# Kernel tuning notes

Hardware: AMD Instinct MI355X
Metric: run time of the kernel (lower is better)

Reference implementation:

```python
import jax, jax.numpy as jnp
import numpy as np

H = 16       # n_heads
DH = 32      # head_dim
LN_EPS = 1e-5


def setup_inputs() -> dict:
    key = jax.random.key(0)
    ks = jax.random.split(key, 10)
    B, N, D, CZ = 1, 768, 512, 128
    sc = 0.05
    return {
        "s": jax.random.normal(ks[0], (B, N, D), jnp.float32),
        "z": jax.random.normal(ks[1], (B, N, N, CZ), jnp.float32),
        "Wq": jax.random.normal(ks[2], (D, D), jnp.float32) * sc,
        "bq": jax.random.normal(ks[3], (D,), jnp.float32) * sc,
        "Wk": jax.random.normal(ks[4], (D, D), jnp.float32) * sc,
        "Wv": jax.random.normal(ks[5], (D, D), jnp.float32) * sc,
        "Wg": jax.random.normal(ks[6], (D, D), jnp.float32) * sc,
        "Wo": jax.random.normal(ks[7], (D, D), jnp.float32) * sc,
        "ln_w": jnp.ones((CZ,), jnp.float32),
        "ln_b": jnp.zeros((CZ,), jnp.float32),
        "Wz": jax.random.normal(ks[8], (H, CZ), jnp.float32) * sc,
    }


def _layernorm(x, w, b):
    mu = jnp.mean(x, axis=-1, keepdims=True)
    var = jnp.var(x, axis=-1, keepdims=True)
    return (x - mu) * jax.lax.rsqrt(var + LN_EPS) * w + b


def reference(s, z, Wq, bq, Wk, Wv, Wg, Wo, ln_w, ln_b, Wz):
    B, N, D = s.shape
    scale = DH ** -0.5
    # fused QKV projections (only q has a bias; k/v bias slots are zero)
    q = (s @ Wq.T + bq).reshape(B, N, H, DH)
    k = (s @ Wk.T).reshape(B, N, H, DH)
    v = (s @ Wv.T).reshape(B, N, H, DH)
    # pair bias: layernorm over c_z then linear c_z -> n_heads, permuted to [B,H,N,N]
    zb = _layernorm(z, ln_w, ln_b) @ Wz.T            # [B,N,N,H]
    bias = jnp.transpose(zb, (0, 3, 1, 2))            # [B,H,N,N]
    logits = jnp.einsum("bqhd,bkhd->bhqk", q, k) * scale + bias
    attn = jax.nn.softmax(logits, axis=-1)
    o = jnp.einsum("bhqk,bkhd->bqhd", attn, v).reshape(B, N, H * DH)
    # sigmoid gate, then output projection
    g = s @ Wg.T
    o = o * jax.nn.sigmoid(g)
    return o @ Wo.T
```

## Files before the change

### kernel.cpp

```cpp
#include <hip/hip_runtime.h>
#include <hip/hip_bf16.h>

#define N_TOK 768
#define D_MODEL 512
#define CZd 128
#define NH 16
#define DHd 32

__global__ __launch_bounds__(256) void bias_kernel(
    const float* __restrict__ z, const float* __restrict__ ln_w,
    const float* __restrict__ ln_b, const float* __restrict__ Wz,
    float* __restrict__ bias)
{
    __shared__ float sWz[NH * CZd];
    __shared__ float swb[2 * CZd];
    __shared__ __align__(16) float sbias[NH][68];
    int t = threadIdx.x;
    for (int i = t; i < NH * CZd; i += 256) sWz[i] = Wz[i];
    if (t < CZd) { swb[t] = ln_w[t]; swb[CZd + t] = ln_b[t]; }
    __syncthreads();

    int q   = blockIdx.y;
    int k0  = blockIdx.x * 64;
    int lane = t & 63;
    int wv   = t >> 6;
    int g    = lane >> 2;
    int sub  = lane & 3;
    int k    = k0 + wv * 16 + g;

    const float* zrow = z + ((size_t)q * N_TOK + k) * CZd;

    float vals[32];
    float sum = 0.f, sumsq = 0.f;
#pragma unroll
    for (int i = 0; i < 8; ++i) {
        float4 v4 = *(const float4*)(zrow + (sub + 4 * i) * 4);
        vals[4*i+0] = v4.x; vals[4*i+1] = v4.y;
        vals[4*i+2] = v4.z; vals[4*i+3] = v4.w;
        sum   += v4.x + v4.y + v4.z + v4.w;
        sumsq += v4.x*v4.x + v4.y*v4.y + v4.z*v4.z + v4.w*v4.w;
    }
    sum   += __shfl_xor(sum, 1);   sum   += __shfl_xor(sum, 2);
    sumsq += __shfl_xor(sumsq, 1); sumsq += __shfl_xor(sumsq, 2);

    float mu   = sum * (1.f / CZd);
    float var  = sumsq * (1.f / CZd) - mu * mu;
    float rstd = rsqrtf(var + 1e-5f);

#pragma unroll
    for (int i = 0; i < 8; ++i) {
#pragma unroll
        for (int jj = 0; jj < 4; ++jj) {
            int e = 16 * i + 4 * sub + jj;
            vals[4*i+jj] = (vals[4*i+jj] - mu) * rstd * swb[e] + swb[CZd + e];
        }
    }

#pragma unroll
    for (int h = 0; h < NH; ++h) {
        float p = 0.f;
#pragma unroll
        for (int i = 0; i < 8; ++i) {
#pragma unroll
            for (int jj = 0; jj < 4; ++jj) {
                int e = 16 * i + 4 * sub + jj;
                p += vals[4*i+jj] * sWz[h * CZd + e];
            }
        }
        p += __shfl_xor(p, 1); p += __shfl_xor(p, 2);
        if ((h & 3) == sub) sbias[h][wv * 16 + g] = p;
    }
    __syncthreads();

    {
        int h  = t >> 4;
        int c4 = t & 15;
        float4 v = *(const float4*)&sbias[h][c4 * 4];
        *(float4*)&bias[((size_t)h * N_TOK + q) * N_TOK + k0 + c4 * 4] = v;
    }
}

#define BKP 32

__global__ __launch_bounds__(256) void qkvg_kernel(
    const float* __restrict__ s,
    const float* __restrict__ Wq, const float* __restrict__ bq,
    const float* __restrict__ Wk, const float* __restrict__ Wv,
    const float* __restrict__ Wg, float* __restrict__ qkvg)
{
    __shared__ __align__(16) float As[BKP][68];
    __shared__ __align__(16) float Bs[BKP][68];
    int t  = threadIdx.x;
    int m0 = blockIdx.y * 64;
    int n0 = blockIdx.x * 64;
    int sel  = n0 >> 9;
    int nloc = n0 & 511;
    const float* W = (sel == 0) ? Wq : (sel == 1) ? Wk : (sel == 2) ? Wv : Wg;

    int tm = t >> 4, tn = t & 15;
    float acc[4][4] = {};

    for (int kt = 0; kt < 512; kt += BKP) {
#pragma unroll
        for (int i = 0; i < 2; ++i) {
            int idx = t + i * 256;
            int row = idx >> 3;
            int c4  = idx & 7;
            float4 a4 = *(const float4*)&s[(size_t)(m0 + row) * 512 + kt + c4 * 4];
            float4 b4 = *(const float4*)&W[(size_t)(nloc + row) * 512 + kt + c4 * 4];
            As[c4*4+0][row] = a4.x; As[c4*4+1][row] = a4.y;
            As[c4*4+2][row] = a4.z; As[c4*4+3][row] = a4.w;
            Bs[c4*4+0][row] = b4.x; Bs[c4*4+1][row] = b4.y;
            Bs[c4*4+2][row] = b4.z; Bs[c4*4+3][row] = b4.w;
        }
        __syncthreads();
#pragma unroll
        for (int kk = 0; kk < BKP; ++kk) {
            float4 a4 = *(const float4*)&As[kk][tm * 4];
            float4 b4 = *(const float4*)&Bs[kk][tn * 4];
            acc[0][0] += a4.x * b4.x; acc[0][1] += a4.x * b4.y;
            acc[0][2] += a4.x * b4.z; acc[0][3] += a4.x * b4.w;
            acc[1][0] += a4.y * b4.x; acc[1][1] += a4.y * b4.y;
            acc[1][2] += a4.y * b4.z; acc[1][3] += a4.y * b4.w;
            acc[2][0] += a4.z * b4.x; acc[2][1] += a4.z * b4.y;
            acc[2][2] += a4.z * b4.z; acc[2][3] += a4.z * b4.w;
            acc[3][0] += a4.w * b4.x; acc[3][1] += a4.w * b4.y;
            acc[3][2] += a4.w * b4.z; acc[3][3] += a4.w * b4.w;
        }
        __syncthreads();
    }

#pragma unroll
    for (int i = 0; i < 4; ++i) {
        int row = m0 + tm * 4 + i;
        float4 v;
        int colb = n0 + tn * 4;
        v.x = acc[i][0]; v.y = acc[i][1]; v.z = acc[i][2]; v.w = acc[i][3];
        if (sel == 0) {
            v.x += bq[colb + 0]; v.y += bq[colb + 1];
            v.z += bq[colb + 2]; v.w += bq[colb + 3];
        }
        *(float4*)&qkvg[(size_t)row * 2048 + colb] = v;
    }
}

#define QT 16
#define KT 64

__global__ __launch_bounds__(256) void attn_kernel(
    const float* __restrict__ qkvg, const float* __restrict__ bias,
    float* __restrict__ o_g)
{
    __shared__ float kt_s[KT][32];
    __shared__ float vt_s[KT][32];
    __shared__ __align__(16) float pt[QT][68];
    __shared__ float mrun[QT], lrun[QT], scalef[QT];

    int t  = threadIdx.x;
    int h  = blockIdx.y;
    int Q0 = blockIdx.x * QT;

    int qi_l = t >> 4;
    int c16  = t & 15;
    int d   = t & 31;
    int qg  = t >> 5;
    int qi0 = qg * 2, qi1 = qg * 2 + 1;

    float4 qreg[8];
    {
        const float* qrow = qkvg + (size_t)(Q0 + qi_l) * 2048 + h * 32;
#pragma unroll
        for (int j = 0; j < 8; ++j) qreg[j] = ((const float4*)qrow)[j];
    }

    float acc0 = 0.f, acc1 = 0.f;
    if (t < QT) { mrun[t] = -1e30f; lrun[t] = 0.f; }
    __syncthreads();

    const float scale = 0.17677669529663687f;

    for (int k0 = 0; k0 < N_TOK; k0 += KT) {
#pragma unroll
        for (int i = 0; i < 2; ++i) {
            int idx = t + i * 256;
            int row = idx >> 3;
            int c4  = idx & 7;
            const float* kp = qkvg + (size_t)(k0 + row) * 2048 +  512 + h * 32 + c4 * 4;
            const float* vp = qkvg + (size_t)(k0 + row) * 2048 + 1024 + h * 32 + c4 * 4;
            float4 k4 = *(const float4*)kp;
            float4 v4 = *(const float4*)vp;
            int sc4 = c4 ^ (row & 7);
            *(float4*)&kt_s[row][sc4 * 4] = k4;
            *(float4*)&vt_s[row][c4 * 4]  = v4;
        }
        __syncthreads();

#pragma unroll
        for (int j = 0; j < 4; ++j) {
            int kk = c16 + 16 * j;
            float dot = 0.f;
#pragma unroll
            for (int c4 = 0; c4 < 8; ++c4) {
                int sc4 = c4 ^ (kk & 7);
                float4 k4 = *(const float4*)&kt_s[kk][sc4 * 4];
                float4 q4 = qreg[c4];
                dot += k4.x*q4.x + k4.y*q4.y + k4.z*q4.z + k4.w*q4.w;
            }
            float b = bias[((size_t)h * N_TOK + (Q0 + qi_l)) * N_TOK + k0 + kk];
            pt[qi_l][kk] = dot * scale + b;
        }
        __syncthreads();

        {
            int lane = t & 63, w = t >> 6;
#pragma unroll
            for (int r4 = 0; r4 < 4; ++r4) {
                int r = w * 4 + r4;
                float x = pt[r][lane];
                float mx = x;
#pragma unroll
                for (int o = 32; o >= 1; o >>= 1) mx = fmaxf(mx, __shfl_xor(mx, o));
                float mold = mrun[r];
                float mnew = fmaxf(mold, mx);
                float p = __expf(x - mnew);
                float ssum = p;
#pragma unroll
                for (int o = 32; o >= 1; o >>= 1) ssum += __shfl_xor(ssum, o);
                pt[r][lane] = p;
                if (lane == 0) {
                    float sc = __expf(mold - mnew);
                    scalef[r] = sc;
                    mrun[r]   = mnew;
                    lrun[r]   = lrun[r] * sc + ssum;
                }
            }
        }
        __syncthreads();

        {
            float s0 = scalef[qi0], s1 = scalef[qi1];
            acc0 *= s0; acc1 *= s1;
#pragma unroll
            for (int kk4 = 0; kk4 < KT; kk4 += 4) {
                float4 p0 = *(const float4*)&pt[qi0][kk4];
                float4 p1 = *(const float4*)&pt[qi1][kk4];
                float v0 = vt_s[kk4+0][d];
                float v1 = vt_s[kk4+1][d];
                float v2 = vt_s[kk4+2][d];
                float v3 = vt_s[kk4+3][d];
                acc0 += p0.x*v0 + p0.y*v1 + p0.z*v2 + p0.w*v3;
                acc1 += p1.x*v0 + p1.y*v1 + p1.z*v2 + p1.w*v3;
            }
        }
        __syncthreads();
    }

    {
        float g0 = qkvg[(size_t)(Q0 + qi0) * 2048 + 1536 + h * 32 + d];
        float g1 = qkvg[(size_t)(Q0 + qi1) * 2048 + 1536 + h * 32 + d];
        float o0 = acc0 / lrun[qi0] / (1.f + __expf(-g0));
        float o1 = acc1 / lrun[qi1] / (1.f + __expf(-g1));
        o_g[(size_t)(Q0 + qi0) * 512 + h * 32 + d] = o0;
        o_g[(size_t)(Q0 + qi1) * 512 + h * 32 + d] = o1;
    }
}

__global__ __launch_bounds__(256) void outproj_kernel(
    const float* __restrict__ o_g, const float* __restrict__ Wo,
    float* __restrict__ out)
{
    __shared__ __align__(16) float As[BKP][68];
    __shared__ __align__(16) float Bs[BKP][68];
    int t  = threadIdx.x;
    int m0 = blockIdx.y * 64;
    int n0 = blockIdx.x * 64;

    int tm = t >> 4, tn = t & 15;
    float acc[4][4] = {};

    for (int kt = 0; kt < 512; kt += BKP) {
#pragma unroll
        for (int i = 0; i < 2; ++i) {
            int idx = t + i * 256;
            int row = idx >> 3;
            int c4  = idx & 7;
            float4 a4 = *(const float4*)&o_g[(size_t)(m0 + row) * 512 + kt + c4 * 4];
            float4 b4 = *(const float4*)&Wo[(size_t)(n0 + row) * 512 + kt + c4 * 4];
            As[c4*4+0][row] = a4.x; As[c4*4+1][row] = a4.y;
            As[c4*4+2][row] = a4.z; As[c4*4+3][row] = a4.w;
            Bs[c4*4+0][row] = b4.x; Bs[c4*4+1][row] = b4.y;
            Bs[c4*4+2][row] = b4.z; Bs[c4*4+3][row] = b4.w;
        }
        __syncthreads();
#pragma unroll
        for (int kk = 0; kk < BKP; ++kk) {
            float4 a4 = *(const float4*)&As[kk][tm * 4];
            float4 b4 = *(const float4*)&Bs[kk][tn * 4];
            acc[0][0] += a4.x * b4.x; acc[0][1] += a4.x * b4.y;
            acc[0][2] += a4.x * b4.z; acc[0][3] += a4.x * b4.w;
            acc[1][0] += a4.y * b4.x; acc[1][1] += a4.y * b4.y;
            acc[1][2] += a4.y * b4.z; acc[1][3] += a4.y * b4.w;
            acc[2][0] += a4.z * b4.x; acc[2][1] += a4.z * b4.y;
            acc[2][2] += a4.z * b4.z; acc[2][3] += a4.z * b4.w;
            acc[3][0] += a4.w * b4.x; acc[3][1] += a4.w * b4.y;
            acc[3][2] += a4.w * b4.z; acc[3][3] += a4.w * b4.w;
        }
        __syncthreads();
    }

#pragma unroll
    for (int i = 0; i < 4; ++i) {
        int row = m0 + tm * 4 + i;
        float4 v;
        v.x = acc[i][0]; v.y = acc[i][1]; v.z = acc[i][2]; v.w = acc[i][3];
        *(float4*)&out[(size_t)row * 512 + n0 + tn * 4] = v;
    }
}

extern "C" void kernel_launch(void* const* d_in, const int* in_sizes, int n_in,
                              void* d_out, int out_size, void* d_ws, size_t ws_size,
                              hipStream_t stream)
{
    const float* s    = (const float*)d_in[0];
    const float* z    = (const float*)d_in[1];
    const float* Wq   = (const float*)d_in[2];
    const float* bq   = (const float*)d_in[3];
    const float* Wk   = (const float*)d_in[4];
    const float* Wv   = (const float*)d_in[5];
    const float* Wg   = (const float*)d_in[6];
    const float* Wo   = (const float*)d_in[7];
    const float* ln_w = (const float*)d_in[8];
    const float* ln_b = (const float*)d_in[9];
    const float* Wz   = (const float*)d_in[10];

    float* ws    = (float*)d_ws;
    float* qkvg  = ws;
    float* biasb = qkvg + (size_t)N_TOK * 2048;
    float* o_g   = biasb + (size_t)NH * N_TOK * N_TOK;
    float* out   = (float*)d_out;

    hipLaunchKernelGGL(qkvg_kernel, dim3(32, 12), dim3(256), 0, stream,
                       s, Wq, bq, Wk, Wv, Wg, qkvg);
    hipLaunchKernelGGL(bias_kernel, dim3(12, 768), dim3(256), 0, stream,
                       z, ln_w, ln_b, Wz, biasb);
    hipLaunchKernelGGL(attn_kernel, dim3(48, 16), dim3(256), 0, stream,
                       qkvg, biasb, o_g);
    hipLaunchKernelGGL(outproj_kernel, dim3(8, 12), dim3(256), 0, stream,
                       o_g, Wo, out);
}
```

Baseline: 575.1 us.

## Process two query rows per bias block and fuse softmax into score pass

The bias kernel now handles two query rows per block, so the Wz and LayerNorm weights staged in shared memory are reused twice and the grid is halved. The Wz dot product now reads float4 from shared memory. In the attention kernel, the online softmax row max and sum are computed in registers with 16-lane shuffles right after the QK dot products, which removes one barrier and a pass over the score tile. The cost is higher register pressure in both kernels, from the doubled vals arrays in the bias kernel.

```diff
diff --git a/kernel.cpp b/kernel.cpp
--- a/kernel.cpp
+++ b/kernel.cpp
@@ -14,13 +14,13 @@
 {
     __shared__ float sWz[NH * CZd];
     __shared__ float swb[2 * CZd];
-    __shared__ __align__(16) float sbias[NH][68];
+    __shared__ __align__(16) float sbias[2][NH][68];
     int t = threadIdx.x;
     for (int i = t; i < NH * CZd; i += 256) sWz[i] = Wz[i];
     if (t < CZd) { swb[t] = ln_w[t]; swb[CZd + t] = ln_b[t]; }
     __syncthreads();
 
-    int q   = blockIdx.y;
+    int q0  = blockIdx.y * 2;
     int k0  = blockIdx.x * 64;
     int lane = t & 63;
     int wv   = t >> 6;
@@ -28,55 +28,68 @@
     int sub  = lane & 3;
     int k    = k0 + wv * 16 + g;
 
-    const float* zrow = z + ((size_t)q * N_TOK + k) * CZd;
-
-    float vals[32];
-    float sum = 0.f, sumsq = 0.f;
+    const float* zrow0 = z + ((size_t)q0 * N_TOK + k) * CZd;
+    const float* zrow1 = zrow0 + (size_t)N_TOK * CZd;
+
+    float vals0[32], vals1[32];
+    float sum0 = 0.f, sq0 = 0.f, sum1 = 0.f, sq1 = 0.f;
 #pragma unroll
     for (int i = 0; i < 8; ++i) {
-        float4 v4 = *(const float4*)(zrow + (sub + 4 * i) * 4);
-        vals[4*i+0] = v4.x; vals[4*i+1] = v4.y;
-        vals[4*i+2] = v4.z; vals[4*i+3] = v4.w;
-        sum   += v4.x + v4.y + v4.z + v4.w;
-        sumsq += v4.x*v4.x + v4.y*v4.y + v4.z*v4.z + v4.w*v4.w;
-    }
-    sum   += __shfl_xor(sum, 1);   sum   += __shfl_xor(sum, 2);
-    sumsq += __shfl_xor(sumsq, 1); sumsq += __shfl_xor(sumsq, 2);
-
-    float mu   = sum * (1.f / CZd);
-    float var  = sumsq * (1.f / CZd) - mu * mu;
-    float rstd = rsqrtf(var + 1e-5f);
+        float4 a = *(const float4*)(zrow0 + (sub + 4 * i) * 4);
+        float4 b = *(const float4*)(zrow1 + (sub + 4 * i) * 4);
+        vals0[4*i+0] = a.x; vals0[4*i+1] = a.y; vals0[4*i+2] = a.z; vals0[4*i+3] = a.w;
+        vals1[4*i+0] = b.x; vals1[4*i+1] = b.y; vals1[4*i+2] = b.z; vals1[4*i+3] = b.w;
+        sum0 += a.x + a.y + a.z + a.w;
+        sq0  += a.x*a.x + a.y*a.y + a.z*a.z + a.w*a.w;
+        sum1 += b.x + b.y + b.z + b.w;
+        sq1  += b.x*b.x + b.y*b.y + b.z*b.z + b.w*b.w;
+    }
+    sum0 += __shfl_xor(sum0, 1); sum0 += __shfl_xor(sum0, 2);
+    sq0  += __shfl_xor(sq0, 1);  sq0  += __shfl_xor(sq0, 2);
+    sum1 += __shfl_xor(sum1, 1); sum1 += __shfl_xor(sum1, 2);
+    sq1  += __shfl_xor(sq1, 1);  sq1  += __shfl_xor(sq1, 2);
+
+    float mu0 = sum0 * (1.f / CZd);
+    float mu1 = sum1 * (1.f / CZd);
+    float rs0 = rsqrtf(sq0 * (1.f / CZd) - mu0 * mu0 + 1e-5f);
+    float rs1 = rsqrtf(sq1 * (1.f / CZd) - mu1 * mu1 + 1e-5f);
 
 #pragma unroll
     for (int i = 0; i < 8; ++i) {
 #pragma unroll
         for (int jj = 0; jj < 4; ++jj) {
             int e = 16 * i + 4 * sub + jj;
-            vals[4*i+jj] = (vals[4*i+jj] - mu) * rstd * swb[e] + swb[CZd + e];
+            float w = swb[e], b = swb[CZd + e];
+            vals0[4*i+jj] = (vals0[4*i+jj] - mu0) * rs0 * w + b;
+            vals1[4*i+jj] = (vals1[4*i+jj] - mu1) * rs1 * w + b;
         }
     }
 
 #pragma unroll
     for (int h = 0; h < NH; ++h) {
-        float p = 0.f;
+        float p0 = 0.f, p1 = 0.f;
 #pragma unroll
         for (int i = 0; i < 8; ++i) {
-#pragma unroll
-            for (int jj = 0; jj < 4; ++jj) {
-                int e = 16 * i + 4 * sub + jj;
-                p += vals[4*i+jj] * sWz[h * CZd + e];
-            }
-        }
-        p += __shfl_xor(p, 1); p += __shfl_xor(p, 2);
-        if ((h & 3) == sub) sbias[h][wv * 16 + g] = p;
+            float4 w4 = *(const float4*)&sWz[h * CZd + 16 * i + 4 * sub];
+            p0 += vals0[4*i+0]*w4.x + vals0[4*i+1]*w4.y + vals0[4*i+2]*w4.z + vals0[4*i+3]*w4.w;
+            p1 += vals1[4*i+0]*w4.x + vals1[4*i+1]*w4.y + vals1[4*i+2]*w4.z + vals1[4*i+3]*w4.w;
+        }
+        p0 += __shfl_xor(p0, 1); p0 += __shfl_xor(p0, 2);
+        p1 += __shfl_xor(p1, 1); p1 += __shfl_xor(p1, 2);
+        if ((h & 3) == sub) {
+            sbias[0][h][wv * 16 + g] = p0;
+            sbias[1][h][wv * 16 + g] = p1;
+        }
     }
     __syncthreads();
 
     {
         int h  = t >> 4;
         int c4 = t & 15;
-        float4 v = *(const float4*)&sbias[h][c4 * 4];
-        *(float4*)&bias[((size_t)h * N_TOK + q) * N_TOK + k0 + c4 * 4] = v;
+        float4 v0 = *(const float4*)&sbias[0][h][c4 * 4];
+        float4 v1 = *(const float4*)&sbias[1][h][c4 * 4];
+        *(float4*)&bias[((size_t)h * N_TOK + q0    ) * N_TOK + k0 + c4 * 4] = v0;
+        *(float4*)&bias[((size_t)h * N_TOK + q0 + 1) * N_TOK + k0 + c4 * 4] = v1;
     }
 }
 
@@ -195,44 +208,45 @@
         }
         __syncthreads();
 
-#pragma unroll
-        for (int j = 0; j < 4; ++j) {
-            int kk = c16 + 16 * j;
-            float dot = 0.f;
-#pragma unroll
-            for (int c4 = 0; c4 < 8; ++c4) {
-                int sc4 = c4 ^ (kk & 7);
-                float4 k4 = *(const float4*)&kt_s[kk][sc4 * 4];
-                float4 q4 = qreg[c4];
-                dot += k4.x*q4.x + k4.y*q4.y + k4.z*q4.z + k4.w*q4.w;
+        {
+            float dots[4];
+#pragma unroll
+            for (int j = 0; j < 4; ++j) {
+                int kk = c16 + 16 * j;
+                float dot = 0.f;
+#pragma unroll
+                for (int c4 = 0; c4 < 8; ++c4) {
+                    int sc4 = c4 ^ (kk & 7);
+                    float4 k4 = *(const float4*)&kt_s[kk][sc4 * 4];
+                    float4 q4 = qreg[c4];
+                    dot += k4.x*q4.x + k4.y*q4.y + k4.z*q4.z + k4.w*q4.w;
+                }
+                float b = bias[((size_t)h * N_TOK + (Q0 + qi_l)) * N_TOK + k0 + kk];
+                dots[j] = dot * scale + b;
             }
-            float b = bias[((size_t)h * N_TOK + (Q0 + qi_l)) * N_TOK + k0 + kk];
-            pt[qi_l][kk] = dot * scale + b;
-        }
-        __syncthreads();
-
-        {
-            int lane = t & 63, w = t >> 6;
-#pragma unroll
-            for (int r4 = 0; r4 < 4; ++r4) {
-                int r = w * 4 + r4;
-                float x = pt[r][lane];
-                float mx = x;
-#pragma unroll
-                for (int o = 32; o >= 1; o >>= 1) mx = fmaxf(mx, __shfl_xor(mx, o));
-                float mold = mrun[r];
-                float mnew = fmaxf(mold, mx);
-                float p = __expf(x - mnew);
-                float ssum = p;
-#pragma unroll
-                for (int o = 32; o >= 1; o >>= 1) ssum += __shfl_xor(ssum, o);
-                pt[r][lane] = p;
-                if (lane == 0) {
-                    float sc = __expf(mold - mnew);
-                    scalef[r] = sc;
-                    mrun[r]   = mnew;
-                    lrun[r]   = lrun[r] * sc + ssum;
-                }
+            float mx = fmaxf(fmaxf(dots[0], dots[1]), fmaxf(dots[2], dots[3]));
+            mx = fmaxf(mx, __shfl_xor(mx, 1));
+            mx = fmaxf(mx, __shfl_xor(mx, 2));
+            mx = fmaxf(mx, __shfl_xor(mx, 4));
+            mx = fmaxf(mx, __shfl_xor(mx, 8));
+            float mold = mrun[qi_l];
+            float mnew = fmaxf(mold, mx);
+            float ssum = 0.f;
+#pragma unroll
+            for (int j = 0; j < 4; ++j) {
+                float p = __expf(dots[j] - mnew);
+                pt[qi_l][c16 + 16 * j] = p;
+                ssum += p;
+            }
+            ssum += __shfl_xor(ssum, 1);
+            ssum += __shfl_xor(ssum, 2);
+            ssum += __shfl_xor(ssum, 4);
+            ssum += __shfl_xor(ssum, 8);
+            if (c16 == 0) {
+                float sc = __expf(mold - mnew);
+                scalef[qi_l] = sc;
+                mrun[qi_l]   = mnew;
+                lrun[qi_l]   = lrun[qi_l] * sc + ssum;
             }
         }
         __syncthreads();
@@ -341,7 +355,7 @@
 
     hipLaunchKernelGGL(qkvg_kernel, dim3(32, 12), dim3(256), 0, stream,
                        s, Wq, bq, Wk, Wv, Wg, qkvg);
-    hipLaunchKernelGGL(bias_kernel, dim3(12, 768), dim3(256), 0, stream,
+    hipLaunchKernelGGL(bias_kernel, dim3(12, 384), dim3(256), 0, stream,
                        z, ln_w, ln_b, Wz, biasb);
     hipLaunchKernelGGL(attn_kernel, dim3(48, 16), dim3(256), 0, stream,
                        qkvg, biasb, o_g);
```

Result: faster. 552.4 us (-3.9%).
